# Optimization experiments

Measured on AMD Instinct MI355X. Metric: run time of the kernel, lower is better.

Reference implementation:

```python
import jax, jax.numpy as jnp
import numpy as np
from jax import lax

P = 16      # GraphBuilder patch size
GROUPS = 8  # GroupNorm groups
EPS = 1e-5


def conv2d(x, w, b):
    y = lax.conv_general_dilated(x, w, (1, 1), 'SAME',
                                 dimension_numbers=('NCHW', 'OIHW', 'NCHW'))
    return y + b[None, :, None, None]


def group_norm(x, g, b):
    B, C, H, W = x.shape
    xr = x.reshape(B, GROUPS, C // GROUPS, H, W)
    m = xr.mean((2, 3, 4), keepdims=True)
    v = xr.var((2, 3, 4), keepdims=True)
    xn = ((xr - m) * lax.rsqrt(v + EPS)).reshape(B, C, H, W)
    return xn * g[None, :, None, None] + b[None, :, None, None]


def grid_edges(gh, gw, B):
    """Bidirectional 4-neighbor grid edges per image, batch-offset. Static (numpy)."""
    idx = np.arange(gh * gw).reshape(gh, gw)
    h = np.stack([idx[:, :-1].ravel(), idx[:, 1:].ravel()])
    v = np.stack([idx[:-1, :].ravel(), idx[1:, :].ravel()])
    e = np.concatenate([h, v, h[::-1], v[::-1]], axis=1)  # [2, E_per]
    offs = (np.arange(B) * (gh * gw))[None, :, None]       # [1, B, 1]
    e = (e[:, None, :] + offs).reshape(2, -1)
    return jnp.asarray(e, dtype=jnp.int32)


def setup_inputs() -> dict:
    key = jax.random.key(0)
    ks = jax.random.split(key, 8)
    B, Cin, H, W, Cout, Td = 16, 32, 256, 256, 32, 256
    s = 0.1
    return dict(
        x=jax.random.normal(ks[0], (B, Cin, H, W), jnp.float32),
        t=jax.random.normal(ks[1], (B, Td), jnp.float32),
        conv_w=jax.random.normal(ks[2], (Cout, Cin, 3, 3), jnp.float32) * s,
        conv_b=jnp.zeros((Cout,), jnp.float32),
        gn_g=jnp.ones((Cout,), jnp.float32),
        gn_b=jnp.zeros((Cout,), jnp.float32),
        gcn_w=jax.random.normal(ks[3], (Cin + 2, Cout), jnp.float32) * s,
        gcn_b=jnp.zeros((Cout,), jnp.float32),
        ln_g=jnp.ones((Cout,), jnp.float32),
        ln_b=jnp.zeros((Cout,), jnp.float32),
        gate_w=jax.random.normal(ks[4], (Cout, 2 * Cout, 3, 3), jnp.float32) * s,
        gate_b=jnp.zeros((Cout,), jnp.float32),
        tp_w=jax.random.normal(ks[5], (2 * Cout, Td), jnp.float32) * s,
        tp_b=jnp.zeros((2 * Cout,), jnp.float32),
    )


def reference(x, t, conv_w, conv_b, gn_g, gn_b, gcn_w, gcn_b,
              ln_g, ln_b, gate_w, gate_b, tp_w, tp_b):
    B, C, H, W = x.shape
    gh, gw = H // P, W // P
    # conv path: Conv3x3 -> GroupNorm(8) -> SiLU
    conv_feat = jax.nn.silu(group_norm(conv2d(x, conv_w, conv_b), gn_g, gn_b))

    # GraphBuilder: per-patch mean features + normalized (row, col) coords
    patch = x.reshape(B, C, gh, P, gw, P).mean((3, 5))          # [B,C,gh,gw]
    yy, xx = jnp.meshgrid(jnp.arange(gh) / gh, jnp.arange(gw) / gw, indexing='ij')
    coords = jnp.broadcast_to(jnp.stack([yy, xx])[None], (B, 2, gh, gw)).astype(x.dtype)
    nodes = jnp.concatenate([patch, coords], 1).transpose(0, 2, 3, 1).reshape(B * gh * gw, C + 2)

    edges = grid_edges(gh, gw, B)
    N = B * gh * gw
    loops = jnp.arange(N, dtype=jnp.int32)
    src = jnp.concatenate([edges[0], loops])
    dst = jnp.concatenate([edges[1], loops])
    deg = jax.ops.segment_sum(jnp.ones_like(src, x.dtype), dst, num_segments=N)
    dinv = lax.rsqrt(deg)
    norm = dinv[src] * dinv[dst]
    h = nodes @ gcn_w                                           # [N, Cout]
    gcn_feat = jax.ops.segment_sum(h[src] * norm[:, None], dst, num_segments=N) + gcn_b

    # LayerNorm over channels
    mu = gcn_feat.mean(-1, keepdims=True)
    var = gcn_feat.var(-1, keepdims=True)
    gcn_feat = (gcn_feat - mu) * lax.rsqrt(var + EPS) * ln_g + ln_b

    Cout = gcn_feat.shape[-1]
    # mirrors torch .view(B, -1, H//16, W//16): row-major reinterpretation
    gcn_feat = gcn_feat.reshape(B, Cout, gh, gw)
    gcn_feat = jax.image.resize(gcn_feat, (B, Cout, H, W), 'bilinear')  # align_corners=False

    combined = jnp.concatenate([conv_feat, gcn_feat], 1)
    gate = jax.nn.sigmoid(conv2d(combined, gate_w, gate_b))
    merged = gate * conv_feat + (1 - gate) * gcn_feat

    tp = t @ tp_w.T + tp_b                                      # [B, 2*Cout]
    gamma, beta = jnp.split(tp.reshape(B, -1, 1, 1), 2, axis=1)
    return merged * (gamma + 1) + beta
```

## Files before the change

kernel.cpp:

```cpp
#include <hip/hip_runtime.h>
#include <hip/hip_bf16.h>
#include <math.h>

typedef __attribute__((ext_vector_type(4))) float f32x4;
typedef __attribute__((ext_vector_type(8))) short s16x8;
typedef __attribute__((ext_vector_type(4))) short s16x4;

static __device__ __forceinline__ float sigmoidf_(float v) { return 1.0f / (1.0f + __expf(-v)); }
static __device__ __forceinline__ unsigned short f2bf(float f) {
  unsigned u = __float_as_uint(f);
  u += 0x7fffu + ((u >> 16) & 1u);
  return (unsigned short)(u >> 16);
}
static __device__ __forceinline__ float bf2f(unsigned short h) {
  return __uint_as_float(((unsigned)h) << 16);
}
static __device__ __forceinline__ s16x4 pk4(float a, float b, float c, float d) {
  union { __hip_bfloat162 h2[2]; s16x4 v; } u;
  u.h2[0] = __float22bfloat162_rn(make_float2(a, b));
  u.h2[1] = __float22bfloat162_rn(make_float2(c, d));
  return u.v;
}
static __device__ __forceinline__ s16x8 pk8(const float* f) {
  union { __hip_bfloat162 h2[4]; s16x8 v; } u;
  u.h2[0] = __float22bfloat162_rn(make_float2(f[0], f[1]));
  u.h2[1] = __float22bfloat162_rn(make_float2(f[2], f[3]));
  u.h2[2] = __float22bfloat162_rn(make_float2(f[4], f[5]));
  u.h2[3] = __float22bfloat162_rn(make_float2(f[6], f[7]));
  return u.v;
}
static __device__ __forceinline__ int xcd_swz(int id) {
  return (id & 7) * 512 + (id >> 3);
}
#define NLOG2E -1.44269504f

__global__ __launch_bounds__(256) void prep_misc(const float* __restrict__ cw,
                                                 const float* __restrict__ gw,
                                                 const float* __restrict__ t,
                                                 const float* __restrict__ tw,
                                                 const float* __restrict__ tb,
                                                 const float* __restrict__ gb,
                                                 unsigned short* __restrict__ wcF,
                                                 unsigned short* __restrict__ wgF,
                                                 float* __restrict__ tpo,
                                                 float* __restrict__ gbs) {
  int blk = blockIdx.x;
  if (blk < 72) {
    int i = blk * 256 + threadIdx.x;
    if (i < 9216) {
      int j = i & 7, lane = (i >> 3) & 63, f = (i >> 9) & 1, tap = i >> 10;
      int o = f * 16 + (lane & 15), c = (lane >> 4) * 8 + j;
      wcF[i] = f2bf(cw[(o * 32 + c) * 9 + tap]);
    }
    if (i < 18432) {
      int j = i & 7, lane = (i >> 3) & 63, f = (i >> 9) & 1;
      int rem = i >> 10;
      int tap = rem % 9, p = rem / 9;
      int o = f * 16 + (lane & 15), ic = p * 32 + (lane >> 4) * 8 + j;
      wgF[i] = f2bf(gw[(o * 64 + ic) * 9 + tap] * NLOG2E);
    }
  } else {
    int idx = (blk - 72) * 256 + threadIdx.x;
    int b = idx >> 6, j = idx & 63;
    const float* tr = t + b * 256;
    const float* wr = tw + j * 256;
    float s = tb[j];
    for (int k = 0; k < 256; ++k) s = fmaf(tr[k], wr[k], s);
    tpo[idx] = s;
    if (blk == 75 && threadIdx.x < 32) gbs[threadIdx.x] = gb[threadIdx.x] * NLOG2E;
  }
}

__global__ __launch_bounds__(512) void conv1_mfma(const float* __restrict__ x,
                                                  const unsigned short* __restrict__ wcF,
                                                  const float* __restrict__ conv_b,
                                                  unsigned short* __restrict__ ycl,
                                                  float* __restrict__ stats,
                                                  float* __restrict__ nodes) {
  __shared__ alignas(16) unsigned short xt[324 * 32];
  __shared__ alignas(16) unsigned short wl[9216];
  int blk = xcd_swz(blockIdx.x);
  int b = blk >> 8, r = blk & 255, gy = r >> 4, gx = r & 15;
  int tid = threadIdx.x;
  int y0 = gy * 16 - 1, x0 = gx * 16 - 1;
  for (int i = tid; i < 1152; i += 512)
    *(s16x8*)&wl[i * 8] = *(const s16x8*)&wcF[i * 8];
  {
    int q = tid >> 6, sl = tid & 63;
    const float* bp = x + ((size_t)(b * 32 + q * 4)) * 65536;
#pragma unroll
    for (int it = 0; it < 6; ++it) {
      int s = sl + it * 64;
      if (s < 324) {
        int row = s / 18, col = s - row * 18;
        int yy = y0 + row, xx = x0 + col;
        float v0 = 0, v1 = 0, v2 = 0, v3 = 0;
        if ((unsigned)yy < 256u && (unsigned)xx < 256u) {
          const float* p = bp + yy * 256 + xx;
          v0 = p[0]; v1 = p[65536]; v2 = p[131072]; v3 = p[196608];
        }
        int slot = (q >> 1) ^ (s & 3) ^ ((s >> 2) & 3);
        *(s16x4*)&xt[s * 32 + slot * 8 + (q & 1) * 4] = pk4(v0, v1, v2, v3);
      }
    }
  }
  __syncthreads();

  int wv = tid >> 6, lane = tid & 63;
  int lr = lane & 15, lg = lane >> 4;

#pragma unroll
  for (int cc = 0; cc < 4; ++cc) {
    int c = wv * 4 + cc;
    int q = c >> 2, jj = c & 3;
    float s = 0.f;
#pragma unroll
    for (int pp = 0; pp < 4; ++pp) {
      int p = pp * 64 + lane;
      int sp = ((p >> 4) + 1) * 18 + (p & 15) + 1;
      int off = sp * 32 + (((q >> 1) ^ (sp & 3) ^ ((sp >> 2) & 3)) << 3) + (q & 1) * 4 + jj;
      s += bf2f(xt[off]);
    }
    for (int m = 1; m < 64; m <<= 1) s += __shfl_xor(s, m);
    if (lane == 0) nodes[(size_t)blk * 34 + c] = s * (1.f / 256.f);
  }
  if (tid == 0) {
    nodes[(size_t)blk * 34 + 32] = (float)gy * (1.f / 16.f);
    nodes[(size_t)blk * 34 + 33] = (float)gx * (1.f / 16.f);
  }

  f32x4 acc[2][2];
  f32x4 cb0 = *(const f32x4*)&conv_b[lg * 4];
  f32x4 cb1 = *(const f32x4*)&conv_b[16 + lg * 4];
#pragma unroll
  for (int mi = 0; mi < 2; ++mi) { acc[mi][0] = cb0; acc[mi][1] = cb1; }
#pragma unroll
  for (int tap = 0; tap < 9; ++tap) {
    s16x8 wf0 = *(const s16x8*)&wl[tap * 1024 + lane * 8];
    s16x8 wf1 = *(const s16x8*)&wl[tap * 1024 + 512 + lane * 8];
    int ky = tap / 3, kx = tap - ky * 3;
#pragma unroll
    for (int mi = 0; mi < 2; ++mi) {
      int s = (wv * 2 + mi + ky) * 18 + lr + kx;
      int offB = s * 32 + ((lg ^ (s & 3) ^ ((s >> 2) & 3)) << 3);
      s16x8 xf = *(const s16x8*)&xt[offB];
      acc[mi][0] = __builtin_amdgcn_mfma_f32_16x16x32_bf16(wf0, xf, acc[mi][0], 0, 0, 0);
      acc[mi][1] = __builtin_amdgcn_mfma_f32_16x16x32_bf16(wf1, xf, acc[mi][1], 0, 0, 0);
    }
  }
#pragma unroll
  for (int mi = 0; mi < 2; ++mi) {
    int oy = gy * 16 + wv * 2 + mi;
    size_t pixbase = ((size_t)b * 65536 + (size_t)oy * 256 + gx * 16 + lr) * 32;
#pragma unroll
    for (int nt = 0; nt < 2; ++nt) {
      f32x4 a = acc[mi][nt];
      *(s16x4*)&ycl[pixbase + nt * 16 + lg * 4] = pk4(a[0], a[1], a[2], a[3]);
    }
  }
  __syncthreads();
  float* gpart = (float*)xt;
#pragma unroll
  for (int nt = 0; nt < 2; ++nt) {
    float s = 0.f, q = 0.f;
#pragma unroll
    for (int mi = 0; mi < 2; ++mi)
#pragma unroll
      for (int rr = 0; rr < 4; ++rr) {
        float v = acc[mi][nt][rr];
        s += v; q += v * v;
      }
    for (int m = 1; m < 16; m <<= 1) { s += __shfl_xor(s, m); q += __shfl_xor(q, m); }
    if (lr == 0) {
      int g = nt * 4 + lg;
      gpart[(g * 2 + 0) * 8 + wv] = s;
      gpart[(g * 2 + 1) * 8 + wv] = q;
    }
  }
  __syncthreads();
  if (tid < 16) {
    int g = tid >> 1, which = tid & 1;
    float v = 0.f;
#pragma unroll
    for (int w = 0; w < 8; ++w) v += gpart[(g * 2 + which) * 8 + w];
    atomicAdd(&stats[(which ? 128 : 0) + b * 8 + g], v);
  }
}

__global__ void gn_finalize(const float* __restrict__ stats,
                            const float* __restrict__ gn_g,
                            const float* __restrict__ gn_b,
                            float* __restrict__ mrs) {
  int i = threadIdx.x;
  int b = i >> 5, c = i & 31, g = c >> 2;
  float s = stats[b * 8 + g], q = stats[128 + b * 8 + g];
  const float n = 262144.f;
  float mean = s / n;
  float var = q / n - mean * mean;
  float rs = rsqrtf(var + 1e-5f);
  float scale = rs * gn_g[c];
  mrs[i] = scale;
  mrs[512 + i] = gn_b[c] - mean * scale;
}

__device__ __forceinline__ float dinv_at(int gy, int gx) {
  return rsqrtf((float)(1 + (gy > 0) + (gy < 15) + (gx > 0) + (gx < 15)));
}

__global__ __launch_bounds__(64) void gcn_fused(const float* __restrict__ nodes,
                                                const float* __restrict__ gw,
                                                const float* __restrict__ gcn_b,
                                                const float* __restrict__ ln_g,
                                                const float* __restrict__ ln_b,
                                                float* __restrict__ lnout) {
  int n = blockIdx.x * 2 + (threadIdx.x >> 5);
  int o = threadIdx.x & 31;
  int r = n & 255, gy = r >> 4, gx = r & 15;
  float dn = dinv_at(gy, gx);
  float s = 0.f;
  {
    const float* nr = nodes + (size_t)n * 34;
    float hh = 0.f;
#pragma unroll
    for (int k = 0; k < 34; ++k) hh = fmaf(nr[k], gw[k * 32 + o], hh);
    s = hh * dn;
  }
  if (gy > 0) {
    const float* nr = nodes + (size_t)(n - 16) * 34;
    float hh = 0.f;
#pragma unroll
    for (int k = 0; k < 34; ++k) hh = fmaf(nr[k], gw[k * 32 + o], hh);
    s += hh * dinv_at(gy - 1, gx);
  }
  if (gy < 15) {
    const float* nr = nodes + (size_t)(n + 16) * 34;
    float hh = 0.f;
#pragma unroll
    for (int k = 0; k < 34; ++k) hh = fmaf(nr[k], gw[k * 32 + o], hh);
    s += hh * dinv_at(gy + 1, gx);
  }
  if (gx > 0) {
    const float* nr = nodes + (size_t)(n - 1) * 34;
    float hh = 0.f;
#pragma unroll
    for (int k = 0; k < 34; ++k) hh = fmaf(nr[k], gw[k * 32 + o], hh);
    s += hh * dinv_at(gy, gx - 1);
  }
  if (gx < 15) {
    const float* nr = nodes + (size_t)(n + 1) * 34;
    float hh = 0.f;
#pragma unroll
    for (int k = 0; k < 34; ++k) hh = fmaf(nr[k], gw[k * 32 + o], hh);
    s += hh * dinv_at(gy, gx + 1);
  }
  float g = dn * s + gcn_b[o];
  float mu = g;
  for (int m = 16; m; m >>= 1) mu += __shfl_xor(mu, m);
  mu *= (1.0f / 32.0f);
  float d = g - mu;
  float v = d * d;
  for (int m = 16; m; m >>= 1) v += __shfl_xor(v, m);
  v *= (1.0f / 32.0f);
  lnout[n * 32 + o] = d * rsqrtf(v + 1e-5f) * ln_g[o] + ln_b[o];
}

__global__ __launch_bounds__(512) void fused_gate_mfma(
    const unsigned short* __restrict__ ycl, const float* __restrict__ mrs,
    const float* __restrict__ lnf, const unsigned short* __restrict__ wgF,
    const float* __restrict__ gbs, const float* __restrict__ tpv,
    float* __restrict__ out) {
  __shared__ alignas(16) unsigned short comb[324 * 40];
  __shared__ alignas(16) unsigned short vvb[18 * 3 * 32];
  __shared__ alignas(16) unsigned short wl[9216];
  int blk = xcd_swz(blockIdx.x);
  int b = blk >> 8, r = blk & 255, gy = r >> 4, gx = r & 15;
  int tid = threadIdx.x;
  int wv = tid >> 6, lane = tid & 63;
  int lr = lane & 15, lg = lane >> 4;
  int y0 = gy * 16 - 1, x0 = gx * 16 - 1;
  const s16x8 z8 = (s16x8){0, 0, 0, 0, 0, 0, 0, 0};

  for (int i = tid; i < 1152; i += 512)
    *(s16x8*)&wl[i * 8] = *(const s16x8*)&wgF[i * 8];

  int row0 = tid / 18, col0 = tid - row0 * 18;
  int yy0_ = y0 + row0, xx0_ = x0 + col0;
  bool act = tid < 324;
  bool in0 = act && ((unsigned)yy0_ < 256u) && ((unsigned)xx0_ < 256u);
  const unsigned short* p0 = ycl + ((size_t)b * 65536 + (size_t)yy0_ * 256 + xx0_) * 32;
  s16x8 v0[4];
#pragma unroll
  for (int h = 0; h < 4; ++h) v0[h] = in0 ? *(const s16x8*)&p0[h * 8] : z8;

  for (int i = tid; i < 1728; i += 512) {
    int row = i / 96, rem = i - row * 96, xc = rem >> 5, c = rem & 31;
    int yy = y0 + row;
    float uy = ((float)yy + 0.5f) * (1.f / 16.f) - 0.5f;
    float fy = floorf(uy);
    float ty = uy - fy;
    int iy0 = (int)fy;
    int iy0c = max(0, iy0), iy1c = min(15, iy0 + 1);
    int gxx = min(15, max(0, gx - 1 + xc));
    const float* base = lnf + (size_t)b * 8192 + c * 256;
    float a0 = base[iy0c * 16 + gxx], a1 = base[iy1c * 16 + gxx];
    vvb[i] = f2bf(a0 + ty * (a1 - a0));
  }

  if (act) {
#pragma unroll
    for (int h = 0; h < 4; ++h) {
      float f0[8];
#pragma unroll
      for (int j = 0; j < 8; ++j) {
        float sc = mrs[b * 32 + h * 8 + j];
        float sh = mrs[512 + b * 32 + h * 8 + j];
        float a = bf2f((unsigned short)v0[h][j]) * sc + sh;
        f0[j] = a * sigmoidf_(a);
      }
      *(s16x8*)&comb[tid * 40 + h * 8] = pk8(f0);
    }
  }
  __syncthreads();

  f32x4 acc[2][2];
  float b0 = gbs[lr], b1 = gbs[16 + lr];
#pragma unroll
  for (int mi = 0; mi < 2; ++mi) {
    acc[mi][0] = (f32x4){b0, b0, b0, b0};
    acc[mi][1] = (f32x4){b1, b1, b1, b1};
  }
#pragma unroll
  for (int tap = 0; tap < 9; ++tap) {
    s16x8 wlo = *(const s16x8*)&wl[tap * 1024 + lane * 8];
    s16x8 whi = *(const s16x8*)&wl[tap * 1024 + 512 + lane * 8];
    int ky = tap / 3, kx = tap - ky * 3;
#pragma unroll
    for (int mi = 0; mi < 2; ++mi) {
      int s = (wv * 2 + mi + ky) * 18 + lr + kx;
      s16x8 a = *(const s16x8*)&comb[s * 40 + lg * 8];
      acc[mi][0] = __builtin_amdgcn_mfma_f32_16x16x32_bf16(a, wlo, acc[mi][0], 0, 0, 0);
      acc[mi][1] = __builtin_amdgcn_mfma_f32_16x16x32_bf16(a, whi, acc[mi][1], 0, 0, 0);
    }
  }

  unsigned cfp[2][2][2];
#pragma unroll
  for (int mi = 0; mi < 2; ++mi) {
    int m = wv * 2 + mi;
#pragma unroll
    for (int nt = 0; nt < 2; ++nt) {
      int oct = nt * 2 + (lr >> 3), el = lr & 7;
#pragma unroll
      for (int rh = 0; rh < 2; ++rh) {
        int px0 = lg * 4 + rh * 2, px1 = px0 + 1;
        int s0 = (m + 1) * 18 + px0 + 1, s1 = (m + 1) * 18 + px1 + 1;
        unsigned lo = comb[s0 * 40 + oct * 8 + el];
        unsigned hi = comb[s1 * 40 + oct * 8 + el];
        cfp[mi][nt][rh] = lo | (hi << 16);
      }
    }
  }
  __syncthreads();

  for (int i = tid; i < 1152; i += 512)
    *(s16x8*)&wl[i * 8] = *(const s16x8*)&wgF[9216 + i * 8];

  if (act) {
    if (((unsigned)yy0_ < 256u) && ((unsigned)xx0_ < 256u)) {
      float ux = ((float)xx0_ + 0.5f) * (1.f / 16.f) - 0.5f;
      float fx = floorf(ux);
      float tx = ux - fx;
      int dx0 = (int)fx - (gx - 1);
      const unsigned short* va = &vvb[(row0 * 3 + dx0) * 32];
      const unsigned short* vb = va + 32;
#pragma unroll
      for (int h = 0; h < 4; ++h) {
        s16x8 av = *(const s16x8*)&va[h * 8];
        s16x8 bv = *(const s16x8*)&vb[h * 8];
        float f[8];
#pragma unroll
        for (int j = 0; j < 8; ++j) {
          float a = bf2f((unsigned short)av[j]);
          f[j] = a + tx * (bf2f((unsigned short)bv[j]) - a);
        }
        *(s16x8*)&comb[tid * 40 + h * 8] = pk8(f);
      }
    } else {
#pragma unroll
      for (int h = 0; h < 4; ++h) *(s16x8*)&comb[tid * 40 + h * 8] = z8;
    }
  }
  __syncthreads();

#pragma unroll
  for (int tap = 0; tap < 9; ++tap) {
    s16x8 wlo = *(const s16x8*)&wl[tap * 1024 + lane * 8];
    s16x8 whi = *(const s16x8*)&wl[tap * 1024 + 512 + lane * 8];
    int ky = tap / 3, kx = tap - ky * 3;
#pragma unroll
    for (int mi = 0; mi < 2; ++mi) {
      int s = (wv * 2 + mi + ky) * 18 + lr + kx;
      s16x8 a = *(const s16x8*)&comb[s * 40 + lg * 8];
      acc[mi][0] = __builtin_amdgcn_mfma_f32_16x16x32_bf16(a, wlo, acc[mi][0], 0, 0, 0);
      acc[mi][1] = __builtin_amdgcn_mfma_f32_16x16x32_bf16(a, whi, acc[mi][1], 0, 0, 0);
    }
  }

#pragma unroll
  for (int mi = 0; mi < 2; ++mi) {
    int m = wv * 2 + mi;
#pragma unroll
    for (int nt = 0; nt < 2; ++nt) {
      int o = nt * 16 + lr;
      int oct = nt * 2 + (lr >> 3), el = lr & 7;
      f32x4 a = acc[mi][nt];
      float gamma = tpv[b * 64 + o] + 1.0f, beta = tpv[b * 64 + 32 + o];
      f32x4 res;
#pragma unroll
      for (int rr = 0; rr < 4; ++rr) {
        int px = lg * 4 + rr;
        int s = (m + 1) * 18 + px + 1;
        unsigned cfu = cfp[mi][nt][rr >> 1];
        float cf = bf2f((unsigned short)((rr & 1) ? (cfu >> 16) : (cfu & 0xffff)));
        float gu = bf2f(comb[s * 40 + oct * 8 + el]);
        float gate = 1.0f / (1.0f + exp2f(a[rr]));
        float merged = gu + gate * (cf - gu);
        res[rr] = merged * gamma + beta;
      }
      *(f32x4*)&out[((size_t)(b * 32 + o)) * 65536 + (size_t)(gy * 16 + m) * 256 + gx * 16 + lg * 4] = res;
    }
  }
}

extern "C" void kernel_launch(void* const* d_in, const int* in_sizes, int n_in,
                              void* d_out, int out_size, void* d_ws, size_t ws_size,
                              hipStream_t stream) {
  const float* x      = (const float*)d_in[0];
  const float* t      = (const float*)d_in[1];
  const float* conv_w = (const float*)d_in[2];
  const float* conv_b = (const float*)d_in[3];
  const float* gn_g   = (const float*)d_in[4];
  const float* gn_b   = (const float*)d_in[5];
  const float* gcn_w  = (const float*)d_in[6];
  const float* gcn_b  = (const float*)d_in[7];
  const float* ln_g   = (const float*)d_in[8];
  const float* ln_b   = (const float*)d_in[9];
  const float* gate_w = (const float*)d_in[10];
  const float* gate_b = (const float*)d_in[11];
  const float* tp_w   = (const float*)d_in[12];
  const float* tp_b   = (const float*)d_in[13];

  float* ws = (float*)d_ws;
  unsigned short* ycl = (unsigned short*)ws;
  float* st    = ws + 16777216;
  float* mrs   = st + 256;
  float* nodes = mrs + 1024;
  float* lnf   = nodes + 139264;
  float* tpv   = lnf + 131072;
  unsigned short* wcF = (unsigned short*)(tpv + 1024);
  unsigned short* wgF = wcF + 9216;
  float* gbs   = (float*)(wgF + 18432);

  hipMemsetAsync(st, 0, 256 * sizeof(float), stream);
  prep_misc<<<76, 256, 0, stream>>>(conv_w, gate_w, t, tp_w, tp_b, gate_b,
                                    wcF, wgF, tpv, gbs);
  conv1_mfma<<<4096, 512, 0, stream>>>(x, wcF, conv_b, ycl, st, nodes);
  gn_finalize<<<1, 512, 0, stream>>>(st, gn_g, gn_b, mrs);
  gcn_fused<<<2048, 64, 0, stream>>>(nodes, gcn_w, gcn_b, ln_g, ln_b, lnf);
  fused_gate_mfma<<<4096, 512, 0, stream>>>(ycl, mrs, lnf, wgF, gbs, tpv,
                                            (float*)d_out);
}
```

Measured before the change: 202.0 us.

## Widen gate-conv tile to 16x32 pixels to halve halo and weight reloads

```diff
diff --git a/kernel.cpp b/kernel.cpp
--- a/kernel.cpp
+++ b/kernel.cpp
@@ -31,6 +31,9 @@
 }
 static __device__ __forceinline__ int xcd_swz(int id) {
   return (id & 7) * 512 + (id >> 3);
+}
+static __device__ __forceinline__ int xcd_swz2(int id) {
+  return (id & 7) * 256 + (id >> 3);
 }
 #define NLOG2E -1.44269504f
 
@@ -264,68 +267,68 @@
   lnout[n * 32 + o] = d * rsqrtf(v + 1e-5f) * ln_g[o] + ln_b[o];
 }
 
-__global__ __launch_bounds__(512) void fused_gate_mfma(
+__global__ __launch_bounds__(512, 4) void fused_gate_mfma(
     const unsigned short* __restrict__ ycl, const float* __restrict__ mrs,
     const float* __restrict__ lnf, const unsigned short* __restrict__ wgF,
     const float* __restrict__ gbs, const float* __restrict__ tpv,
     float* __restrict__ out) {
-  __shared__ alignas(16) unsigned short comb[324 * 40];
-  __shared__ alignas(16) unsigned short vvb[18 * 3 * 32];
+  __shared__ alignas(16) unsigned short comb[612 * 40];
+  __shared__ alignas(16) unsigned short vvb[18 * 4 * 32];
   __shared__ alignas(16) unsigned short wl[9216];
-  int blk = xcd_swz(blockIdx.x);
-  int b = blk >> 8, r = blk & 255, gy = r >> 4, gx = r & 15;
+  int blk = xcd_swz2(blockIdx.x);
+  int b = blk >> 7, r = blk & 127, gy = r >> 3, gp = r & 7;
   int tid = threadIdx.x;
   int wv = tid >> 6, lane = tid & 63;
   int lr = lane & 15, lg = lane >> 4;
-  int y0 = gy * 16 - 1, x0 = gx * 16 - 1;
+  int y0 = gy * 16 - 1, x0 = gp * 32 - 1;
   const s16x8 z8 = (s16x8){0, 0, 0, 0, 0, 0, 0, 0};
 
   for (int i = tid; i < 1152; i += 512)
     *(s16x8*)&wl[i * 8] = *(const s16x8*)&wgF[i * 8];
 
-  int row0 = tid / 18, col0 = tid - row0 * 18;
-  int yy0_ = y0 + row0, xx0_ = x0 + col0;
-  bool act = tid < 324;
-  bool in0 = act && ((unsigned)yy0_ < 256u) && ((unsigned)xx0_ < 256u);
-  const unsigned short* p0 = ycl + ((size_t)b * 65536 + (size_t)yy0_ * 256 + xx0_) * 32;
-  s16x8 v0[4];
-#pragma unroll
-  for (int h = 0; h < 4; ++h) v0[h] = in0 ? *(const s16x8*)&p0[h * 8] : z8;
-
-  for (int i = tid; i < 1728; i += 512) {
-    int row = i / 96, rem = i - row * 96, xc = rem >> 5, c = rem & 31;
-    int yy = y0 + row;
+  for (int i = tid; i < 2304; i += 512) {
+    int hr = i >> 7, rem = i & 127, xc = rem >> 5, c = rem & 31;
+    int yy = y0 + hr;
     float uy = ((float)yy + 0.5f) * (1.f / 16.f) - 0.5f;
     float fy = floorf(uy);
     float ty = uy - fy;
     int iy0 = (int)fy;
     int iy0c = max(0, iy0), iy1c = min(15, iy0 + 1);
-    int gxx = min(15, max(0, gx - 1 + xc));
+    int gc = min(15, max(0, 2 * gp - 1 + xc));
     const float* base = lnf + (size_t)b * 8192 + c * 256;
-    float a0 = base[iy0c * 16 + gxx], a1 = base[iy1c * 16 + gxx];
+    float a0 = base[iy0c * 16 + gc], a1 = base[iy1c * 16 + gc];
     vvb[i] = f2bf(a0 + ty * (a1 - a0));
   }
 
-  if (act) {
-#pragma unroll
-    for (int h = 0; h < 4; ++h) {
-      float f0[8];
-#pragma unroll
-      for (int j = 0; j < 8; ++j) {
-        float sc = mrs[b * 32 + h * 8 + j];
-        float sh = mrs[512 + b * 32 + h * 8 + j];
-        float a = bf2f((unsigned short)v0[h][j]) * sc + sh;
-        f0[j] = a * sigmoidf_(a);
-      }
-      *(s16x8*)&comb[tid * 40 + h * 8] = pk8(f0);
-    }
-  }
-  __syncthreads();
-
-  f32x4 acc[2][2];
+  for (int s = tid; s < 612; s += 512) {
+    int hr = s / 34, hc = s - hr * 34;
+    int yy = y0 + hr, xx = x0 + hc;
+    if (((unsigned)yy < 256u) && ((unsigned)xx < 256u)) {
+      const unsigned short* p = ycl + ((size_t)b * 65536 + (size_t)yy * 256 + xx) * 32;
+#pragma unroll
+      for (int h = 0; h < 4; ++h) {
+        s16x8 v = *(const s16x8*)&p[h * 8];
+        float f0[8];
+#pragma unroll
+        for (int j = 0; j < 8; ++j) {
+          float sc = mrs[b * 32 + h * 8 + j];
+          float sh = mrs[512 + b * 32 + h * 8 + j];
+          float a = bf2f((unsigned short)v[j]) * sc + sh;
+          f0[j] = a * sigmoidf_(a);
+        }
+        *(s16x8*)&comb[s * 40 + h * 8] = pk8(f0);
+      }
+    } else {
+#pragma unroll
+      for (int h = 0; h < 4; ++h) *(s16x8*)&comb[s * 40 + h * 8] = z8;
+    }
+  }
+  __syncthreads();
+
+  f32x4 acc[4][2];
   float b0 = gbs[lr], b1 = gbs[16 + lr];
 #pragma unroll
-  for (int mi = 0; mi < 2; ++mi) {
+  for (int mi = 0; mi < 4; ++mi) {
     acc[mi][0] = (f32x4){b0, b0, b0, b0};
     acc[mi][1] = (f32x4){b1, b1, b1, b1};
   }
@@ -335,25 +338,27 @@
     s16x8 whi = *(const s16x8*)&wl[tap * 1024 + 512 + lane * 8];
     int ky = tap / 3, kx = tap - ky * 3;
 #pragma unroll
-    for (int mi = 0; mi < 2; ++mi) {
-      int s = (wv * 2 + mi + ky) * 18 + lr + kx;
+    for (int mi = 0; mi < 4; ++mi) {
+      int q = wv * 4 + mi, r_ = q >> 1, ch = q & 1;
+      int s = (r_ + ky) * 34 + ch * 16 + lr + kx;
       s16x8 a = *(const s16x8*)&comb[s * 40 + lg * 8];
       acc[mi][0] = __builtin_amdgcn_mfma_f32_16x16x32_bf16(a, wlo, acc[mi][0], 0, 0, 0);
       acc[mi][1] = __builtin_amdgcn_mfma_f32_16x16x32_bf16(a, whi, acc[mi][1], 0, 0, 0);
     }
   }
 
-  unsigned cfp[2][2][2];
-#pragma unroll
-  for (int mi = 0; mi < 2; ++mi) {
-    int m = wv * 2 + mi;
+  unsigned cfp[4][2][2];
+#pragma unroll
+  for (int mi = 0; mi < 4; ++mi) {
+    int q = wv * 4 + mi, r_ = q >> 1, ch = q & 1;
 #pragma unroll
     for (int nt = 0; nt < 2; ++nt) {
       int oct = nt * 2 + (lr >> 3), el = lr & 7;
 #pragma unroll
       for (int rh = 0; rh < 2; ++rh) {
         int px0 = lg * 4 + rh * 2, px1 = px0 + 1;
-        int s0 = (m + 1) * 18 + px0 + 1, s1 = (m + 1) * 18 + px1 + 1;
+        int s0 = (r_ + 1) * 34 + ch * 16 + px0 + 1;
+        int s1 = (r_ + 1) * 34 + ch * 16 + px1 + 1;
         unsigned lo = comb[s0 * 40 + oct * 8 + el];
         unsigned hi = comb[s1 * 40 + oct * 8 + el];
         cfp[mi][nt][rh] = lo | (hi << 16);
@@ -365,13 +370,15 @@
   for (int i = tid; i < 1152; i += 512)
     *(s16x8*)&wl[i * 8] = *(const s16x8*)&wgF[9216 + i * 8];
 
-  if (act) {
-    if (((unsigned)yy0_ < 256u) && ((unsigned)xx0_ < 256u)) {
-      float ux = ((float)xx0_ + 0.5f) * (1.f / 16.f) - 0.5f;
+  for (int s = tid; s < 612; s += 512) {
+    int hr = s / 34, hc = s - hr * 34;
+    int yy = y0 + hr, xx = x0 + hc;
+    if (((unsigned)yy < 256u) && ((unsigned)xx < 256u)) {
+      float ux = ((float)xx + 0.5f) * (1.f / 16.f) - 0.5f;
       float fx = floorf(ux);
       float tx = ux - fx;
-      int dx0 = (int)fx - (gx - 1);
-      const unsigned short* va = &vvb[(row0 * 3 + dx0) * 32];
+      int dx0 = (int)fx - (2 * gp - 1);
+      const unsigned short* va = &vvb[(hr * 4 + dx0) * 32];
       const unsigned short* vb = va + 32;
 #pragma unroll
       for (int h = 0; h < 4; ++h) {
@@ -383,11 +390,11 @@
           float a = bf2f((unsigned short)av[j]);
           f[j] = a + tx * (bf2f((unsigned short)bv[j]) - a);
         }
-        *(s16x8*)&comb[tid * 40 + h * 8] = pk8(f);
+        *(s16x8*)&comb[s * 40 + h * 8] = pk8(f);
       }
     } else {
 #pragma unroll
-      for (int h = 0; h < 4; ++h) *(s16x8*)&comb[tid * 40 + h * 8] = z8;
+      for (int h = 0; h < 4; ++h) *(s16x8*)&comb[s * 40 + h * 8] = z8;
     }
   }
   __syncthreads();
@@ -398,8 +405,9 @@
     s16x8 whi = *(const s16x8*)&wl[tap * 1024 + 512 + lane * 8];
     int ky = tap / 3, kx = tap - ky * 3;
 #pragma unroll
-    for (int mi = 0; mi < 2; ++mi) {
-      int s = (wv * 2 + mi + ky) * 18 + lr + kx;
+    for (int mi = 0; mi < 4; ++mi) {
+      int q = wv * 4 + mi, r_ = q >> 1, ch = q & 1;
+      int s = (r_ + ky) * 34 + ch * 16 + lr + kx;
       s16x8 a = *(const s16x8*)&comb[s * 40 + lg * 8];
       acc[mi][0] = __builtin_amdgcn_mfma_f32_16x16x32_bf16(a, wlo, acc[mi][0], 0, 0, 0);
       acc[mi][1] = __builtin_amdgcn_mfma_f32_16x16x32_bf16(a, whi, acc[mi][1], 0, 0, 0);
@@ -407,8 +415,9 @@
   }
 
 #pragma unroll
-  for (int mi = 0; mi < 2; ++mi) {
-    int m = wv * 2 + mi;
+  for (int mi = 0; mi < 4; ++mi) {
+    int q = wv * 4 + mi, r_ = q >> 1, ch = q & 1;
+    int oy = gy * 16 + r_;
 #pragma unroll
     for (int nt = 0; nt < 2; ++nt) {
       int o = nt * 16 + lr;
@@ -419,7 +428,7 @@
 #pragma unroll
       for (int rr = 0; rr < 4; ++rr) {
         int px = lg * 4 + rr;
-        int s = (m + 1) * 18 + px + 1;
+        int s = (r_ + 1) * 34 + ch * 16 + px + 1;
         unsigned cfu = cfp[mi][nt][rr >> 1];
         float cf = bf2f((unsigned short)((rr & 1) ? (cfu >> 16) : (cfu & 0xffff)));
         float gu = bf2f(comb[s * 40 + oct * 8 + el]);
@@ -427,7 +436,7 @@
         float merged = gu + gate * (cf - gu);
         res[rr] = merged * gamma + beta;
       }
-      *(f32x4*)&out[((size_t)(b * 32 + o)) * 65536 + (size_t)(gy * 16 + m) * 256 + gx * 16 + lg * 4] = res;
+      *(f32x4*)&out[((size_t)(b * 32 + o)) * 65536 + (size_t)oy * 256 + gp * 32 + ch * 16 + lg * 4] = res;
     }
   }
 }
@@ -467,6 +476,6 @@
   conv1_mfma<<<4096, 512, 0, stream>>>(x, wcF, conv_b, ycl, st, nodes);
   gn_finalize<<<1, 512, 0, stream>>>(st, gn_g, gn_b, mrs);
   gcn_fused<<<2048, 64, 0, stream>>>(nodes, gcn_w, gcn_b, ln_g, ln_b, lnf);
-  fused_gate_mfma<<<4096, 512, 0, stream>>>(ycl, mrs, lnf, wgF, gbs, tpv,
+  fused_gate_mfma<<<2048, 512, 0, stream>>>(ycl, mrs, lnf, wgF, gbs, tpv,
                                             (float*)d_out);
 }
```

Result: no change. 203.1 us (+0.6%).
